# Kernel tuning notes

Hardware: AMD Instinct MI355X
Metric: run time of the kernel (lower is better)

## Reference

```python
import jax, jax.numpy as jnp
import numpy as np

B, C, S, Q = 4, 3, 5, 5
E = 90 * 768          # encoding_size for encoding_method != 1
N1 = B * C * S        # 60 support rows
N2 = B * C * Q        # 60 query rows
H = 32                # width of every Dense layer


def setup_inputs() -> dict:
    key = jax.random.key(0)
    ks = jax.random.split(key, 20)
    p = lambda k, shape: jax.random.normal(k, shape, jnp.float32) * 0.1
    return {
        "support_distance": jax.random.normal(ks[0], (N1, E), jnp.float32),
        "support_label": jax.random.randint(ks[1], (B, 15), 0, C, jnp.int32),
        "query_distance": jax.random.normal(ks[2], (N2, E), jnp.float32),
        # fvc_bar / gvc_bar (shared between distance and label paths)
        "W_fvc_bar": p(ks[3], (1, H)),  "b_fvc_bar": p(ks[4], (H,)),
        "W_gvc_bar": p(ks[5], (H, H)), "b_gvc_bar": p(ks[6], (H,)),
        # fu / gu (input to fu is concat([repeat(32-dim), 1-dim]) -> 33)
        "W_fu": p(ks[7], (H + 1, H)),  "b_fu": p(ks[8], (H,)),
        "W_gu": p(ks[9], (H, H)),      "b_gu": p(ks[10], (H,)),
        # fvc / gvc
        "W_fvc": p(ks[11], (H + 1, H)), "b_fvc": p(ks[12], (H,)),
        "W_gvc": p(ks[13], (H, H)),     "b_gvc": p(ks[14], (H,)),
        # fz / gz
        "W_fz": p(ks[15], (H + 1, H)),  "b_fz": p(ks[16], (H,)),
        "W_gz": p(ks[17], (H, H)),      "b_gz": p(ks[18], (H,)),
    }


def reference(support_distance, support_label, query_distance,
              W_fvc_bar, b_fvc_bar, W_gvc_bar, b_gvc_bar,
              W_fu, b_fu, W_gu, b_gu,
              W_fvc, b_fvc, W_gvc, b_gvc,
              W_fz, b_fz, W_gz, b_gz):
    relu = jax.nn.relu
    d1 = support_distance[..., None]                                   # [N1,E,1]
    # v_bar: fvc_bar over each scalar of the distance, mean over rows, then gvc_bar
    v_bar = relu(jnp.mean(relu(d1 @ W_fvc_bar + b_fvc_bar), axis=0)
                 @ W_gvc_bar + b_gvc_bar)                               # [E,32]
    # c_bar: same stack applied to one-hot labels
    lab = jax.nn.one_hot(support_label.reshape(N1).astype(jnp.int32), C)[..., None]  # [N1,C,1]
    c_bar = relu(jnp.mean(relu(lab @ W_fvc_bar + b_fvc_bar), axis=0)
                 @ W_gvc_bar + b_gvc_bar)                               # [C,32]
    # fu on concat([repeat(v_bar), d1]): split the 33-row weight to avoid concat
    Wu_v, wu_d = W_fu[:H], W_fu[H:]                                     # [32,32],[1,32]
    alpha = jnp.mean(relu((v_bar @ Wu_v)[None] + d1 * wu_d[0] + b_fu), axis=1)  # [N1,32]
    beta = jnp.mean(relu((c_bar @ Wu_v)[None] + lab * wu_d[0] + b_fu), axis=1)  # [N1,32]
    u_n = relu((alpha + beta) @ W_gu + b_gu)                            # [N1,32]
    # fvc on concat([repeat(u_n over E), d1]), mean over rows, gvc
    Wv_u, wv_d = W_fvc[:H], W_fvc[H:]
    v = relu(jnp.mean(relu((u_n @ Wv_u)[:, None, :] + d1 * wv_d[0] + b_fvc),
                      axis=0) @ W_gvc + b_gvc)                          # [E,32]
    # query branch: fz on concat([repeat(v), d2]), mean over E, gz
    d2 = query_distance[..., None]                                      # [N2,E,1]
    Wz_v, wz_d = W_fz[:H], W_fz[H:]
    z = jnp.mean(relu((v @ Wz_v)[None] + d2 * wz_d[0] + b_fz), axis=1)  # [N2,32]
    new_distance = relu(z @ W_gz + b_gz)                                # [N2,32]
    return new_distance.reshape(B, C, Q, H)
```

## Files before the change

kernel.cpp:

```cpp
#include <hip/hip_runtime.h>

#define E_DIM 69120
#define N1 60
#define H 32
#define CC 3
#define TEB 64
#define NB2 (E_DIM / TEB)
#define SDS 68
#define SBA 34
#define SBT 68
#define PSZ (N1 * H)

typedef float f2 __attribute__((ext_vector_type(2)));

__device__ __forceinline__ f2 relu_fma2(f2 a, f2 b, f2 c) {
    return __builtin_elementwise_max(__builtin_elementwise_fma(a, b, c), (f2)(0.f));
}


template<bool ATOMIC>
__global__ __launch_bounds__(512, 4) void kA23(
    const float* __restrict__ d,
    const float* __restrict__ Wfvb, const float* __restrict__ bfvb,
    const float* __restrict__ Wgvb, const float* __restrict__ bgvb,
    const float* __restrict__ Wfu,  const float* __restrict__ bfu,
    float* __restrict__ outp)
{
    __shared__ __align__(16) float ds[N1 * SDS];
    __shared__ __align__(16) float bufA[64 * SBA];
    __shared__ __align__(16) float bufB[64 * SBA];
    float* bufT = bufA;
    const int tid = threadIdx.x;
    const long sE = (long)blockIdx.x * TEB;

    for (int i = tid; i < N1 * (TEB / 4); i += 512) {
        const int n = i >> 4, c = (i & 15) * 4;
        *(float4*)(ds + n * SDS + c) = *(const float4*)(d + (long)n * E_DIM + sE + c);
    }
    __syncthreads();

    const int eL = tid & 63;
    const int h0 = __builtin_amdgcn_readfirstlane((tid >> 6) * 4);

    {
        f2 wf[2], bf[2], ta[2], tb[2];
        #pragma unroll
        for (int q = 0; q < 2; ++q) {
            wf[q] = f2{Wfvb[h0 + 2*q] * (1.f/N1), Wfvb[h0 + 2*q + 1] * (1.f/N1)};
            bf[q] = f2{bfvb[h0 + 2*q] * (1.f/N1), bfvb[h0 + 2*q + 1] * (1.f/N1)};
            ta[q] = (f2)(0.f); tb[q] = (f2)(0.f);
        }
        const float* dp = ds + eL;
        #pragma unroll 5
        for (int n = 0; n < N1; n += 2) {
            const float dv0 = dp[n * SDS];
            const float dv1 = dp[(n + 1) * SDS];
            const f2 d02 = f2{dv0, dv0}, d12 = f2{dv1, dv1};
            #pragma unroll
            for (int q = 0; q < 2; ++q) {
                ta[q] += relu_fma2(d02, wf[q], bf[q]);
                tb[q] += relu_fma2(d12, wf[q], bf[q]);
            }
        }
        #pragma unroll
        for (int q = 0; q < 2; ++q)
            *(f2*)(bufA + eL * SBA + h0 + 2*q) = ta[q] + tb[q];
    }
    __syncthreads();

    {
        f2 acc[2];
        #pragma unroll
        for (int q = 0; q < 2; ++q) acc[q] = f2{bgvb[h0 + 2*q], bgvb[h0 + 2*q + 1]};
        #pragma unroll
        for (int k = 0; k < H; ++k) {
            const float t = bufA[eL * SBA + k];
            const f2 t2 = f2{t, t};
            #pragma unroll
            for (int q = 0; q < 2; ++q)
                acc[q] = __builtin_elementwise_fma(t2, *(const f2*)(Wgvb + k * H + h0 + 2*q), acc[q]);
        }
        #pragma unroll
        for (int q = 0; q < 2; ++q)
            *(f2*)(bufB + eL * SBA + h0 + 2*q) = __builtin_elementwise_max(acc[q], (f2)(0.f));
    }
    __syncthreads();

    {
        f2 acc[2];
        #pragma unroll
        for (int q = 0; q < 2; ++q) acc[q] = f2{bfu[h0 + 2*q], bfu[h0 + 2*q + 1]};
        #pragma unroll
        for (int k = 0; k < H; ++k) {
            const float t = bufB[eL * SBA + k];
            const f2 t2 = f2{t, t};
            #pragma unroll
            for (int q = 0; q < 2; ++q)
                acc[q] = __builtin_elementwise_fma(t2, *(const f2*)(Wfu + k * H + h0 + 2*q), acc[q]);
        }
        #pragma unroll
        for (int q = 0; q < 2; ++q) {
            bufT[(h0 + 2*q)     * SBT + eL] = acc[q].x;
            bufT[(h0 + 2*q + 1) * SBT + eL] = acc[q].y;
        }
    }
    __syncthreads();

    {
        const int hl = tid & 31;
        const int bn = ((tid >> 6) << 3) + ((tid >> 5) & 1) * 4;
        if (bn < N1) {
            const float wv = Wfu[H * H + hl];
            const f2 wv2 = f2{wv, wv};
            f2 acc2[4];
            #pragma unroll
            for (int i = 0; i < 4; ++i) acc2[i] = (f2)(0.f);
            const float* dr = ds + bn * SDS;
            #pragma unroll 2
            for (int e4 = 0; e4 < TEB; e4 += 4) {
                const float4 w4 = *(const float4*)(bufT + hl * SBT + e4);
                const f2 wa = f2{w4.x, w4.y}, wb = f2{w4.z, w4.w};
                #pragma unroll
                for (int i = 0; i < 4; ++i) {
                    const float4 di = *(const float4*)(dr + i * SDS + e4);
                    acc2[i] += relu_fma2(f2{di.x, di.y}, wv2, wa)
                             + relu_fma2(f2{di.z, di.w}, wv2, wb);
                }
            }
            if (ATOMIC) {
                #pragma unroll
                for (int i = 0; i < 4; ++i) atomicAdd(&outp[(bn + i) * H + hl], acc2[i].x + acc2[i].y);
            } else {
                float* base = outp + (long)blockIdx.x * PSZ;
                #pragma unroll
                for (int i = 0; i < 4; ++i) base[(bn + i) * H + hl] = acc2[i].x + acc2[i].y;
            }
        }
    }
}

template<bool ATOMIC>
__global__ __launch_bounds__(512, 4) void kCf23(
    const float* __restrict__ d, const float* __restrict__ d2,
    const float* __restrict__ uwb,
    const float* __restrict__ Wfvc,
    const float* __restrict__ Wgvc, const float* __restrict__ bgvc,
    const float* __restrict__ Wfz,  const float* __restrict__ bfz,
    float* __restrict__ outp)
{
    __shared__ __align__(16) float ds[N1 * SDS];
    __shared__ __align__(16) float bufA[64 * SBA];
    __shared__ __align__(16) float bufB[64 * SBA];
    float* bufT = bufA;
    float* u_l  = bufB;
    const int tid = threadIdx.x;
    const long sE = (long)blockIdx.x * TEB;

    for (int i = tid; i < N1 * (TEB / 4); i += 512) {
        const int n = i >> 4, c = (i & 15) * 4;
        *(float4*)(ds + n * SDS + c) = *(const float4*)(d + (long)n * E_DIM + sE + c);
    }
    if (tid < PSZ / 4) {
        float4 u = ((const float4*)uwb)[tid];
        u.x *= (1.f / N1); u.y *= (1.f / N1); u.z *= (1.f / N1); u.w *= (1.f / N1);
        ((float4*)u_l)[tid] = u;
    }
    __syncthreads();

    const int eL = tid & 63;
    const int h0 = __builtin_amdgcn_readfirstlane((tid >> 6) * 4);

    {
        f2 wvd[2], ma[2], mb[2];
        #pragma unroll
        for (int q = 0; q < 2; ++q) {
            wvd[q] = f2{Wfvc[H * H + h0 + 2*q] * (1.f/N1), Wfvc[H * H + h0 + 2*q + 1] * (1.f/N1)};
            ma[q] = (f2)(0.f); mb[q] = (f2)(0.f);
        }
        const float* dp = ds + eL;
        #pragma unroll 5
        for (int n = 0; n < N1; n += 2) {
            const float dv0 = dp[n * SDS];
            const float dv1 = dp[(n + 1) * SDS];
            const f2 d02 = f2{dv0, dv0}, d12 = f2{dv1, dv1};
            #pragma unroll
            for (int q = 0; q < 2; ++q) {
                const f2 u0 = *(const f2*)(u_l + n * H + h0 + 2*q);
                const f2 u1 = *(const f2*)(u_l + (n + 1) * H + h0 + 2*q);
                ma[q] += relu_fma2(d02, wvd[q], u0);
                mb[q] += relu_fma2(d12, wvd[q], u1);
            }
        }
        #pragma unroll
        for (int q = 0; q < 2; ++q)
            *(f2*)(bufA + eL * SBA + h0 + 2*q) = ma[q] + mb[q];
    }
    __syncthreads();

    float4 q0, q1;
    {
        const int n0 = tid >> 4, c0 = (tid & 15) * 4;
        q0 = *(const float4*)(d2 + (long)n0 * E_DIM + sE + c0);
        if (tid < 448) {
            const int i1 = tid + 512, n1 = i1 >> 4, c1 = (i1 & 15) * 4;
            q1 = *(const float4*)(d2 + (long)n1 * E_DIM + sE + c1);
        }
    }

    {
        f2 acc[2];
        #pragma unroll
        for (int q = 0; q < 2; ++q) acc[q] = f2{bgvc[h0 + 2*q], bgvc[h0 + 2*q + 1]};
        #pragma unroll
        for (int k = 0; k < H; ++k) {
            const float t = bufA[eL * SBA + k];
            const f2 t2 = f2{t, t};
            #pragma unroll
            for (int q = 0; q < 2; ++q)
                acc[q] = __builtin_elementwise_fma(t2, *(const f2*)(Wgvc + k * H + h0 + 2*q), acc[q]);
        }
        #pragma unroll
        for (int q = 0; q < 2; ++q)
            *(f2*)(bufB + eL * SBA + h0 + 2*q) = __builtin_elementwise_max(acc[q], (f2)(0.f));
    }

    {
        const int n0 = tid >> 4, c0 = (tid & 15) * 4;
        *(float4*)(ds + n0 * SDS + c0) = q0;
        if (tid < 448) {
            const int i1 = tid + 512, n1 = i1 >> 4, c1 = (i1 & 15) * 4;
            *(float4*)(ds + n1 * SDS + c1) = q1;
        }
    }
    __syncthreads();

    {
        f2 acc[2];
        #pragma unroll
        for (int q = 0; q < 2; ++q) acc[q] = f2{bfz[h0 + 2*q], bfz[h0 + 2*q + 1]};
        #pragma unroll
        for (int k = 0; k < H; ++k) {
            const float t = bufB[eL * SBA + k];
            const f2 t2 = f2{t, t};
            #pragma unroll
            for (int q = 0; q < 2; ++q)
                acc[q] = __builtin_elementwise_fma(t2, *(const f2*)(Wfz + k * H + h0 + 2*q), acc[q]);
        }
        #pragma unroll
        for (int q = 0; q < 2; ++q) {
            bufT[(h0 + 2*q)     * SBT + eL] = acc[q].x;
            bufT[(h0 + 2*q + 1) * SBT + eL] = acc[q].y;
        }
    }
    __syncthreads();

    {
        const int hl = tid & 31;
        const int bn = ((tid >> 6) << 3) + ((tid >> 5) & 1) * 4;
        if (bn < N1) {
            const float wv = Wfz[H * H + hl];
            const f2 wv2 = f2{wv, wv};
            f2 acc2[4];
            #pragma unroll
            for (int i = 0; i < 4; ++i) acc2[i] = (f2)(0.f);
            const float* dr = ds + bn * SDS;
            #pragma unroll 2
            for (int e4 = 0; e4 < TEB; e4 += 4) {
                const float4 w4 = *(const float4*)(bufT + hl * SBT + e4);
                const f2 wa = f2{w4.x, w4.y}, wb = f2{w4.z, w4.w};
                #pragma unroll
                for (int i = 0; i < 4; ++i) {
                    const float4 di = *(const float4*)(dr + i * SDS + e4);
                    acc2[i] += relu_fma2(f2{di.x, di.y}, wv2, wa)
                             + relu_fma2(f2{di.z, di.w}, wv2, wb);
                }
            }
            if (ATOMIC) {
                #pragma unroll
                for (int i = 0; i < 4; ++i) atomicAdd(&outp[(bn + i) * H + hl], acc2[i].x + acc2[i].y);
            } else {
                float* base = outp + (long)blockIdx.x * PSZ;
                #pragma unroll
                for (int i = 0; i < 4; ++i) base[(bn + i) * H + hl] = acc2[i].x + acc2[i].y;
            }
        }
    }
}

__global__ __launch_bounds__(256) void kR(
    const float* __restrict__ part, float* __restrict__ out)
{
    __shared__ float red[16][17];
    const int tid = threadIdx.x;
    const int oLoc = tid & 15, c = tid >> 4;
    const int o = blockIdx.x * 16 + oLoc;
    const int b0 = c * 68;
    const int bN = (NB2 - b0 < 68) ? (NB2 - b0) : 68;
    const float* p = part + (long)b0 * PSZ + o;
    float s = 0.f;
    #pragma unroll 4
    for (int b = 0; b < bN; ++b) s += p[(long)b * PSZ];
    red[c][oLoc] = s;
    __syncthreads();
    if (tid < 16) {
        float t = 0.f;
        #pragma unroll
        for (int ci = 0; ci < 16; ++ci) t += red[ci][tid];
        out[blockIdx.x * 16 + tid] = t;
    }
}

__global__ __launch_bounds__(1024) void kB(
    const float* __restrict__ alphaAcc, const int* __restrict__ label,
    const float* __restrict__ Wfvb, const float* __restrict__ bfvb,
    const float* __restrict__ Wgvb, const float* __restrict__ bgvb,
    const float* __restrict__ Wfu,  const float* __restrict__ bfu,
    const float* __restrict__ Wgu,  const float* __restrict__ bgu,
    const float* __restrict__ Wfvc, const float* __restrict__ bfvc,
    float* __restrict__ uwb)
{
    __shared__ float up_l[N1 * H];
    __shared__ float un_l[N1 * H];
    __shared__ float cb_l[CC * H];
    __shared__ float cw_l[CC * H];
    __shared__ int   cnt[CC];
    const int tid = threadIdx.x;

    if (tid < CC) cnt[tid] = 0;
    __syncthreads();
    if (tid < N1) atomicAdd(&cnt[label[tid]], 1);
    __syncthreads();

    if (tid < CC * H) {
        const int c = tid / H, h = tid % H;
        const float nc = (float)cnt[c];
        float s = bgvb[h];
        #pragma unroll
        for (int k = 0; k < H; ++k) {
            const float t1c = (nc * fmaxf(Wfvb[k] + bfvb[k], 0.f) +
                               ((float)N1 - nc) * fmaxf(bfvb[k], 0.f)) * (1.f / N1);
            s = fmaf(t1c, Wgvb[k * H + h], s);
        }
        cb_l[tid] = fmaxf(s, 0.f);
    }
    __syncthreads();
    if (tid < CC * H) {
        const int c = tid / H, h = tid % H;
        float s = bfu[h];
        #pragma unroll
        for (int k = 0; k < H; ++k) s = fmaf(cb_l[c * H + k], Wfu[k * H + h], s);
        cw_l[tid] = s;
    }
    __syncthreads();
    for (int t = tid; t < N1 * H; t += 1024) {
        const int n = t >> 5, h = t & 31;
        const int ln = label[n];
        const float wud = Wfu[H * H + h];
        float s = 0.f;
        #pragma unroll
        for (int c = 0; c < CC; ++c)
            s += fmaxf(cw_l[c * H + h] + ((c == ln) ? wud : 0.f), 0.f);
        up_l[t] = alphaAcc[t] * (1.f / E_DIM) + s * (1.f / CC);
    }
    __syncthreads();
    for (int t = tid; t < N1 * H; t += 1024) {
        const int n = t >> 5, h = t & 31;
        float s = bgu[h];
        #pragma unroll
        for (int k = 0; k < H; ++k) s = fmaf(up_l[n * H + k], Wgu[k * H + h], s);
        un_l[t] = fmaxf(s, 0.f);
    }
    __syncthreads();
    for (int t = tid; t < N1 * H; t += 1024) {
        const int n = t >> 5, h = t & 31;
        float s = bfvc[h];
        #pragma unroll
        for (int k = 0; k < H; ++k) s = fmaf(un_l[n * H + k], Wfvc[k * H + h], s);
        uwb[t] = s;
    }
}

__global__ __launch_bounds__(1024) void kD(
    const float* __restrict__ zAcc,
    const float* __restrict__ Wgz, const float* __restrict__ bgz,
    float* __restrict__ out)
{
    __shared__ float z_l[N1 * H];
    const int tid = threadIdx.x;
    for (int t = tid; t < N1 * H; t += 1024) z_l[t] = zAcc[t] * (1.f / E_DIM);
    __syncthreads();
    for (int t = tid; t < N1 * H; t += 1024) {
        const int n = t >> 5, h = t & 31;
        float s = bgz[h];
        #pragma unroll
        for (int k = 0; k < H; ++k) s = fmaf(z_l[n * H + k], Wgz[k * H + h], s);
        out[t] = fmaxf(s, 0.f);
    }
}

extern "C" void kernel_launch(void* const* d_in, const int* in_sizes, int n_in,
                              void* d_out, int out_size, void* d_ws, size_t ws_size,
                              hipStream_t stream)
{
    const float* sup  = (const float*)d_in[0];
    const int*   lab  = (const int*)d_in[1];
    const float* qry  = (const float*)d_in[2];
    const float* Wfvb = (const float*)d_in[3];
    const float* bfvb = (const float*)d_in[4];
    const float* Wgvb = (const float*)d_in[5];
    const float* bgvb = (const float*)d_in[6];
    const float* Wfu  = (const float*)d_in[7];
    const float* bfu  = (const float*)d_in[8];
    const float* Wgu  = (const float*)d_in[9];
    const float* bgu  = (const float*)d_in[10];
    const float* Wfvc = (const float*)d_in[11];
    const float* bfvc = (const float*)d_in[12];
    const float* Wgvc = (const float*)d_in[13];
    const float* bgvc = (const float*)d_in[14];
    const float* Wfz  = (const float*)d_in[15];
    const float* bfz  = (const float*)d_in[16];
    const float* Wgz  = (const float*)d_in[17];
    const float* bgz  = (const float*)d_in[18];
    float* out = (float*)d_out;

    float* alphaAcc = (float*)d_ws;
    float* zAcc     = alphaAcc + PSZ;
    float* uwb      = zAcc + PSZ;
    float* partA    = uwb + PSZ;
    float* partZ    = partA + (size_t)NB2 * PSZ;

    const size_t needMain = (3 * (size_t)PSZ + 2 * (size_t)NB2 * PSZ) * sizeof(float);

    if (ws_size >= needMain) {
        kA23<false><<<NB2, 512, 0, stream>>>(sup, Wfvb, bfvb, Wgvb, bgvb, Wfu, bfu, partA);
        kR<<<PSZ / 16, 256, 0, stream>>>(partA, alphaAcc);
        kB<<<1, 1024, 0, stream>>>(alphaAcc, lab, Wfvb, bfvb, Wgvb, bgvb, Wfu, bfu,
                                   Wgu, bgu, Wfvc, bfvc, uwb);
        kCf23<false><<<NB2, 512, 0, stream>>>(sup, qry, uwb, Wfvc, Wgvc, bgvc, Wfz, bfz, partZ);
        kR<<<PSZ / 16, 256, 0, stream>>>(partZ, zAcc);
        kD<<<1, 1024, 0, stream>>>(zAcc, Wgz, bgz, out);
    } else {
        (void)hipMemsetAsync(alphaAcc, 0, 2 * PSZ * sizeof(float), stream);
        kA23<true><<<NB2, 512, 0, stream>>>(sup, Wfvb, bfvb, Wgvb, bgvb, Wfu, bfu, alphaAcc);
        kB<<<1, 1024, 0, stream>>>(alphaAcc, lab, Wfvb, bfvb, Wgvb, bgvb, Wfu, bfu,
                                   Wgu, bgu, Wfvc, bfvc, uwb);
        kCf23<true><<<NB2, 512, 0, stream>>>(sup, qry, uwb, Wfvc, Wgvc, bgvc, Wfz, bfz, zAcc);
        kD<<<1, 1024, 0, stream>>>(zAcc, Wgz, bgz, out);
    }
}
```

Before: 85.50 us.

## Fuse partial-sum reductions with tail kernels via last-block atomic counter

Merges each cross-block reduction kernel with the single-block follow-up kernel (kB or kD) that consumed its output. The last reduction block, found with an atomic counter plus thread fences, runs the small MLP tail itself. This removes two kernel launches and the gaps between them from the six-launch sequence. In exchange it relies on counters reset inside kA23, and a single 256-thread block now does the tail work that a 1024-thread block did before.

Result: slower. 103.0 us (+20.4%).

```diff
diff --git a/kernel.cpp b/kernel.cpp
--- a/kernel.cpp
+++ b/kernel.cpp
@@ -10,6 +10,7 @@
 #define SBA 34
 #define SBT 68
 #define PSZ (N1 * H)
+#define NRB 120
 
 typedef float f2 __attribute__((ext_vector_type(2)));
 
@@ -24,7 +25,7 @@
     const float* __restrict__ Wfvb, const float* __restrict__ bfvb,
     const float* __restrict__ Wgvb, const float* __restrict__ bgvb,
     const float* __restrict__ Wfu,  const float* __restrict__ bfu,
-    float* __restrict__ outp)
+    float* __restrict__ outp, int* __restrict__ ctr)
 {
     __shared__ __align__(16) float ds[N1 * SDS];
     __shared__ __align__(16) float bufA[64 * SBA];
@@ -32,6 +33,8 @@
     float* bufT = bufA;
     const int tid = threadIdx.x;
     const long sE = (long)blockIdx.x * TEB;
+
+    if (!ATOMIC && blockIdx.x == 0 && tid == 0) { ctr[0] = 0; ctr[1] = 0; }
 
     for (int i = tid; i < N1 * (TEB / 4); i += 512) {
         const int n = i >> 4, c = (i & 15) * 4;
@@ -287,26 +290,147 @@
     }
 }
 
-__global__ __launch_bounds__(256) void kR(
-    const float* __restrict__ part, float* __restrict__ out)
+__global__ __launch_bounds__(256) void kRB(
+    const float* __restrict__ part, float* __restrict__ alphaAcc,
+    int* __restrict__ ctr, const int* __restrict__ label,
+    const float* __restrict__ Wfvb, const float* __restrict__ bfvb,
+    const float* __restrict__ Wgvb, const float* __restrict__ bgvb,
+    const float* __restrict__ Wfu,  const float* __restrict__ bfu,
+    const float* __restrict__ Wgu,  const float* __restrict__ bgu,
+    const float* __restrict__ Wfvc, const float* __restrict__ bfvc,
+    float* __restrict__ uwb)
 {
     __shared__ float red[16][17];
+    __shared__ float up_l[PSZ];
+    __shared__ float un_l[PSZ];
+    __shared__ float cb_l[CC * H];
+    __shared__ float cw_l[CC * H];
+    __shared__ int   cnt[CC];
+    __shared__ int   isLast;
     const int tid = threadIdx.x;
-    const int oLoc = tid & 15, c = tid >> 4;
-    const int o = blockIdx.x * 16 + oLoc;
-    const int b0 = c * 68;
-    const int bN = (NB2 - b0 < 68) ? (NB2 - b0) : 68;
-    const float* p = part + (long)b0 * PSZ + o;
-    float s = 0.f;
-    #pragma unroll 4
-    for (int b = 0; b < bN; ++b) s += p[(long)b * PSZ];
-    red[c][oLoc] = s;
-    __syncthreads();
-    if (tid < 16) {
-        float t = 0.f;
-        #pragma unroll
-        for (int ci = 0; ci < 16; ++ci) t += red[ci][tid];
-        out[blockIdx.x * 16 + tid] = t;
+
+    {
+        const int oLoc = tid & 15, c = tid >> 4;
+        const int o = blockIdx.x * 16 + oLoc;
+        const int b0 = c * 68;
+        const int bN = (NB2 - b0 < 68) ? (NB2 - b0) : 68;
+        const float* p = part + (long)b0 * PSZ + o;
+        float s = 0.f;
+        #pragma unroll 4
+        for (int b = 0; b < bN; ++b) s += p[(long)b * PSZ];
+        red[c][oLoc] = s;
+        __syncthreads();
+        if (tid < 16) {
+            float t = 0.f;
+            #pragma unroll
+            for (int ci = 0; ci < 16; ++ci) t += red[ci][tid];
+            alphaAcc[blockIdx.x * 16 + tid] = t;
+        }
+    }
+    __threadfence();
+    __syncthreads();
+    if (tid == 0) isLast = (atomicAdd(&ctr[0], 1) == NRB - 1);
+    __syncthreads();
+    if (!isLast) return;
+    __threadfence();
+
+    if (tid < CC) cnt[tid] = 0;
+    __syncthreads();
+    if (tid < N1) atomicAdd(&cnt[label[tid]], 1);
+    __syncthreads();
+    if (tid < CC * H) {
+        const int c = tid / H, h = tid % H;
+        const float nc = (float)cnt[c];
+        float s = bgvb[h];
+        #pragma unroll
+        for (int k = 0; k < H; ++k) {
+            const float t1c = (nc * fmaxf(Wfvb[k] + bfvb[k], 0.f) +
+                               ((float)N1 - nc) * fmaxf(bfvb[k], 0.f)) * (1.f / N1);
+            s = fmaf(t1c, Wgvb[k * H + h], s);
+        }
+        cb_l[tid] = fmaxf(s, 0.f);
+    }
+    __syncthreads();
+    if (tid < CC * H) {
+        const int c = tid / H, h = tid % H;
+        float s = bfu[h];
+        #pragma unroll
+        for (int k = 0; k < H; ++k) s = fmaf(cb_l[c * H + k], Wfu[k * H + h], s);
+        cw_l[tid] = s;
+    }
+    __syncthreads();
+    for (int t = tid; t < PSZ; t += 256) {
+        const int n = t >> 5, h = t & 31;
+        const int ln = label[n];
+        const float wud = Wfu[H * H + h];
+        float s = 0.f;
+        #pragma unroll
+        for (int c = 0; c < CC; ++c)
+            s += fmaxf(cw_l[c * H + h] + ((c == ln) ? wud : 0.f), 0.f);
+        up_l[t] = alphaAcc[t] * (1.f / E_DIM) + s * (1.f / CC);
+    }
+    __syncthreads();
+    for (int t = tid; t < PSZ; t += 256) {
+        const int n = t >> 5, h = t & 31;
+        float s = bgu[h];
+        #pragma unroll
+        for (int k = 0; k < H; ++k) s = fmaf(up_l[n * H + k], Wgu[k * H + h], s);
+        un_l[t] = fmaxf(s, 0.f);
+    }
+    __syncthreads();
+    for (int t = tid; t < PSZ; t += 256) {
+        const int n = t >> 5, h = t & 31;
+        float s = bfvc[h];
+        #pragma unroll
+        for (int k = 0; k < H; ++k) s = fmaf(un_l[n * H + k], Wfvc[k * H + h], s);
+        uwb[t] = s;
+    }
+}
+
+__global__ __launch_bounds__(256) void kRD(
+    const float* __restrict__ part, float* __restrict__ zAcc,
+    int* __restrict__ ctr,
+    const float* __restrict__ Wgz, const float* __restrict__ bgz,
+    float* __restrict__ out)
+{
+    __shared__ float red[16][17];
+    __shared__ float z_l[PSZ];
+    __shared__ int   isLast;
+    const int tid = threadIdx.x;
+
+    {
+        const int oLoc = tid & 15, c = tid >> 4;
+        const int o = blockIdx.x * 16 + oLoc;
+        const int b0 = c * 68;
+        const int bN = (NB2 - b0 < 68) ? (NB2 - b0) : 68;
+        const float* p = part + (long)b0 * PSZ + o;
+        float s = 0.f;
+        #pragma unroll 4
+        for (int b = 0; b < bN; ++b) s += p[(long)b * PSZ];
+        red[c][oLoc] = s;
+        __syncthreads();
+        if (tid < 16) {
+            float t = 0.f;
+            #pragma unroll
+            for (int ci = 0; ci < 16; ++ci) t += red[ci][tid];
+            zAcc[blockIdx.x * 16 + tid] = t;
+        }
+    }
+    __threadfence();
+    __syncthreads();
+    if (tid == 0) isLast = (atomicAdd(&ctr[1], 1) == NRB - 1);
+    __syncthreads();
+    if (!isLast) return;
+    __threadfence();
+
+    for (int t = tid; t < PSZ; t += 256) z_l[t] = zAcc[t] * (1.f / E_DIM);
+    __syncthreads();
+    for (int t = tid; t < PSZ; t += 256) {
+        const int n = t >> 5, h = t & 31;
+        float s = bgz[h];
+        #pragma unroll
+        for (int k = 0; k < H; ++k) s = fmaf(z_l[n * H + k], Wgz[k * H + h], s);
+        out[t] = fmaxf(s, 0.f);
     }
 }
 
@@ -330,7 +454,6 @@
     __syncthreads();
     if (tid < N1) atomicAdd(&cnt[label[tid]], 1);
     __syncthreads();
-
     if (tid < CC * H) {
         const int c = tid / H, h = tid % H;
         const float nc = (float)cnt[c];
@@ -428,20 +551,20 @@
     float* uwb      = zAcc + PSZ;
     float* partA    = uwb + PSZ;
     float* partZ    = partA + (size_t)NB2 * PSZ;
-
-    const size_t needMain = (3 * (size_t)PSZ + 2 * (size_t)NB2 * PSZ) * sizeof(float);
+    int*   ctr      = (int*)(partZ + (size_t)NB2 * PSZ);
+
+    const size_t needMain = (3 * (size_t)PSZ + 2 * (size_t)NB2 * PSZ) * sizeof(float) + 2 * sizeof(int);
 
     if (ws_size >= needMain) {
-        kA23<false><<<NB2, 512, 0, stream>>>(sup, Wfvb, bfvb, Wgvb, bgvb, Wfu, bfu, partA);
-        kR<<<PSZ / 16, 256, 0, stream>>>(partA, alphaAcc);
-        kB<<<1, 1024, 0, stream>>>(alphaAcc, lab, Wfvb, bfvb, Wgvb, bgvb, Wfu, bfu,
-                                   Wgu, bgu, Wfvc, bfvc, uwb);
+        kA23<false><<<NB2, 512, 0, stream>>>(sup, Wfvb, bfvb, Wgvb, bgvb, Wfu, bfu, partA, ctr);
+        kRB<<<NRB, 256, 0, stream>>>(partA, alphaAcc, ctr, lab,
+                                     Wfvb, bfvb, Wgvb, bgvb, Wfu, bfu,
+                                     Wgu, bgu, Wfvc, bfvc, uwb);
         kCf23<false><<<NB2, 512, 0, stream>>>(sup, qry, uwb, Wfvc, Wgvc, bgvc, Wfz, bfz, partZ);
-        kR<<<PSZ / 16, 256, 0, stream>>>(partZ, zAcc);
-        kD<<<1, 1024, 0, stream>>>(zAcc, Wgz, bgz, out);
+        kRD<<<NRB, 256, 0, stream>>>(partZ, zAcc, ctr, Wgz, bgz, out);
     } else {
         (void)hipMemsetAsync(alphaAcc, 0, 2 * PSZ * sizeof(float), stream);
-        kA23<true><<<NB2, 512, 0, stream>>>(sup, Wfvb, bfvb, Wgvb, bgvb, Wfu, bfu, alphaAcc);
+        kA23<true><<<NB2, 512, 0, stream>>>(sup, Wfvb, bfvb, Wgvb, bgvb, Wfu, bfu, alphaAcc, nullptr);
         kB<<<1, 1024, 0, stream>>>(alphaAcc, lab, Wfvb, bfvb, Wgvb, bgvb, Wfu, bfu,
                                    Wgu, bgu, Wfvc, bfvc, uwb);
         kCf23<true><<<NB2, 512, 0, stream>>>(sup, qry, uwb, Wfvc, Wgvc, bgvc, Wfz, bfz, zAcc);
```
